# Performance work log

Hardware: AMD Instinct MI355X
Metric: run time of the kernel (lower is better)

The kernel has to match this reference:

```python
import jax, jax.numpy as jnp
import numpy as np


def setup_inputs() -> dict:
    key = jax.random.key(0)
    k1, k2, k3 = jax.random.split(key, 3)
    x = jax.random.normal(k1, (8, 3, 256, 256), dtype=jnp.float32)
    conv_w = jax.random.normal(k2, (64, 3), dtype=jnp.float32)  # 1x1 conv weight [O, C]
    w = jax.random.normal(k3, (64, 8), dtype=jnp.float32)       # per-channel LBP weights
    return {"x": x, "conv_w": conv_w, "w": w}


def _heaviside(d):
    # torch.heaviside(d, 0.): 1 where d > 0, else 0 (including d == 0)
    return jnp.where(d > 0, jnp.ones((), d.dtype), jnp.zeros((), d.dtype))


def reference(x, conv_w, w):
    # 1x1 conv, no bias: [N,C,H,W] x [O,C] -> [N,O,H,W]
    y = jnp.einsum('nchw,oc->nohw', x, conv_w)
    c = y[:, :, 1:-1, 1:-1]  # center, [N,O,H-2,W-2]
    # 8 neighbor shifts in the original order
    shifts = [
        y[:, :, 0:-2, 0:-2], y[:, :, 0:-2, 1:-1], y[:, :, 0:-2, 2:],
        y[:, :, 1:-1, 0:-2], y[:, :, 2:, 0:-2], y[:, :, 2:, 1:-1],
        y[:, :, 2:, 2:],    y[:, :, 1:-1, 2:],
    ]
    act = jnp.stack([_heaviside(c - s) for s in shifts], axis=2)  # [N,O,8,H-2,W-2]
    # weighted reduction over the 8 directions with exp(w)
    x_cat = jnp.einsum('nolhw,ol->nohw', act, jnp.exp(w))
    padded = jnp.pad(x_cat, ((0, 0), (0, 0), (1, 1), (1, 1)))  # ZeroPad2d(1)
    # res=True: concat raw input along channels -> [N, 3+O, H, W]
    return jnp.concatenate([x, padded], axis=1)
```

## Files before the change

kernel.cpp:

```cpp
#include <hip/hip_runtime.h>


__global__ __launch_bounds__(256) void lbp_all(
    const float* __restrict__ x,
    const float* __restrict__ conv_w,
    const float* __restrict__ w,
    float* __restrict__ out)
{
#pragma clang fp contract(off)
    const int n     = blockIdx.z;
    const int og    = blockIdx.y;
    const int tid   = threadIdx.x;
    const int lane  = tid & 63;
    const int wv    = tid >> 6;
    const int col   = lane * 4;
    const int hrow0 = blockIdx.x * 8 + wv * 2;

    __shared__ float ews[128];
    if (tid < 128) ews[tid] = expf(w[og * 128 + tid]);

    const float* xn = x + (size_t)n * 3 * 65536;

    float4 xr[4][3];
    #pragma unroll
    for (int r = 0; r < 4; ++r) {
        int row = hrow0 - 1 + r;
        row = row < 0 ? 0 : (row > 255 ? 255 : row);
        #pragma unroll
        for (int ch = 0; ch < 3; ++ch)
            xr[r][ch] = *(const float4*)(xn + (ch * 256 + row) * 256 + col);
    }

    if (og == 0) {
        #pragma unroll
        for (int ch = 0; ch < 3; ++ch) {
            float* cp = out + ((((size_t)n * 67 + ch) * 256 + hrow0) * 256 + col);
            *(float4*)cp         = xr[1][ch];
            *(float4*)(cp + 256) = xr[2][ch];
        }
    }

    __syncthreads();

    float* obase = out + ((((size_t)n * 67 + 3 + og * 16) * 256 + hrow0) * 256 + col);

    #pragma unroll 4
    for (int oi = 0; oi < 16; ++oi) {
        const int o = og * 16 + oi;
        const float cw0 = conv_w[o * 3 + 0];
        const float cw1 = conv_w[o * 3 + 1];
        const float cw2 = conv_w[o * 3 + 2];

        float Y[4][6];
        #pragma unroll
        for (int r = 0; r < 4; ++r) {
            float4 yv;
            yv.x = xr[r][0].x * cw0 + xr[r][1].x * cw1 + xr[r][2].x * cw2;
            yv.y = xr[r][0].y * cw0 + xr[r][1].y * cw1 + xr[r][2].y * cw2;
            yv.z = xr[r][0].z * cw0 + xr[r][1].z * cw1 + xr[r][2].z * cw2;
            yv.w = xr[r][0].w * cw0 + xr[r][1].w * cw1 + xr[r][2].w * cw2;
            Y[r][1] = yv.x; Y[r][2] = yv.y; Y[r][3] = yv.z; Y[r][4] = yv.w;
            Y[r][0] = __shfl_up(yv.w, 1);
            Y[r][5] = __shfl_down(yv.x, 1);
        }

        const float e0 = ews[oi * 8 + 0], e1 = ews[oi * 8 + 1];
        const float e2 = ews[oi * 8 + 2], e3 = ews[oi * 8 + 3];
        const float e4 = ews[oi * 8 + 4], e5 = ews[oi * 8 + 5];
        const float e6 = ews[oi * 8 + 6], e7 = ews[oi * 8 + 7];

        #pragma unroll
        for (int k = 0; k < 2; ++k) {
            const int hrow = hrow0 + k;
            float res[4];
            if (hrow == 0 || hrow == 255) {
                res[0] = res[1] = res[2] = res[3] = 0.f;
            } else {
                const float* up  = Y[k];
                const float* mid = Y[k + 1];
                const float* dn  = Y[k + 2];
                #pragma unroll
                for (int j = 0; j < 4; ++j) {
                    const float c = mid[j + 1];
                    float acc;
                    acc  = (c > up [j    ]) ? e0 : 0.f;
                    acc += (c > up [j + 1]) ? e1 : 0.f;
                    acc += (c > up [j + 2]) ? e2 : 0.f;
                    acc += (c > mid[j    ]) ? e3 : 0.f;
                    acc += (c > dn [j    ]) ? e4 : 0.f;
                    acc += (c > dn [j + 1]) ? e5 : 0.f;
                    acc += (c > dn [j + 2]) ? e6 : 0.f;
                    acc += (c > mid[j + 2]) ? e7 : 0.f;
                    res[j] = acc;
                }
                if (lane == 0)  res[0] = 0.f;
                if (lane == 63) res[3] = 0.f;
            }
            *(float4*)(obase + (size_t)oi * 65536 + (size_t)k * 256) =
                make_float4(res[0], res[1], res[2], res[3]);
        }
    }
}

extern "C" void kernel_launch(void* const* d_in, const int* in_sizes, int n_in,
                              void* d_out, int out_size, void* d_ws, size_t ws_size,
                              hipStream_t stream) {
    const float* x      = (const float*)d_in[0];
    const float* conv_w = (const float*)d_in[1];
    const float* w      = (const float*)d_in[2];
    float* out          = (float*)d_out;

    dim3 grid(32, 4, 8);
    dim3 block(256);
    hipLaunchKernelGGL(lbp_all, grid, block, 0, stream, x, conv_w, w, out);
}
```

Before: 152.0 us.

## Use nontemporal stores, halo loads instead of shuffles, and tune unroll/occupancy

```diff
diff --git a/kernel.cpp b/kernel.cpp
--- a/kernel.cpp
+++ b/kernel.cpp
@@ -1,7 +1,9 @@
 #include <hip/hip_runtime.h>
 
 
-__global__ __launch_bounds__(256) void lbp_all(
+typedef float vfloat4 __attribute__((ext_vector_type(4)));
+
+__global__ __launch_bounds__(256, 4) void lbp_all(
     const float* __restrict__ x,
     const float* __restrict__ conv_w,
     const float* __restrict__ w,
@@ -20,23 +22,30 @@
     if (tid < 128) ews[tid] = expf(w[og * 128 + tid]);
 
     const float* xn = x + (size_t)n * 3 * 65536;
+    const int cl = (col == 0)   ? 0   : col - 1;
+    const int cr = (col == 252) ? 255 : col + 4;
 
-    float4 xr[4][3];
+    vfloat4 xr[4][3];
+    float   hl[4][3], hr[4][3];
     #pragma unroll
     for (int r = 0; r < 4; ++r) {
         int row = hrow0 - 1 + r;
         row = row < 0 ? 0 : (row > 255 ? 255 : row);
         #pragma unroll
-        for (int ch = 0; ch < 3; ++ch)
-            xr[r][ch] = *(const float4*)(xn + (ch * 256 + row) * 256 + col);
+        for (int ch = 0; ch < 3; ++ch) {
+            const float* bp = xn + (ch * 256 + row) * 256;
+            xr[r][ch] = *(const vfloat4*)(bp + col);
+            hl[r][ch] = bp[cl];
+            hr[r][ch] = bp[cr];
+        }
     }
 
     if (og == 0) {
         #pragma unroll
         for (int ch = 0; ch < 3; ++ch) {
             float* cp = out + ((((size_t)n * 67 + ch) * 256 + hrow0) * 256 + col);
-            *(float4*)cp         = xr[1][ch];
-            *(float4*)(cp + 256) = xr[2][ch];
+            __builtin_nontemporal_store(xr[1][ch], (vfloat4*)cp);
+            __builtin_nontemporal_store(xr[2][ch], (vfloat4*)(cp + 256));
         }
     }
 
@@ -44,7 +53,7 @@
 
     float* obase = out + ((((size_t)n * 67 + 3 + og * 16) * 256 + hrow0) * 256 + col);
 
-    #pragma unroll 4
+    #pragma unroll 2
     for (int oi = 0; oi < 16; ++oi) {
         const int o = og * 16 + oi;
         const float cw0 = conv_w[o * 3 + 0];
@@ -54,20 +63,18 @@
         float Y[4][6];
         #pragma unroll
         for (int r = 0; r < 4; ++r) {
-            float4 yv;
-            yv.x = xr[r][0].x * cw0 + xr[r][1].x * cw1 + xr[r][2].x * cw2;
-            yv.y = xr[r][0].y * cw0 + xr[r][1].y * cw1 + xr[r][2].y * cw2;
-            yv.z = xr[r][0].z * cw0 + xr[r][1].z * cw1 + xr[r][2].z * cw2;
-            yv.w = xr[r][0].w * cw0 + xr[r][1].w * cw1 + xr[r][2].w * cw2;
-            Y[r][1] = yv.x; Y[r][2] = yv.y; Y[r][3] = yv.z; Y[r][4] = yv.w;
-            Y[r][0] = __shfl_up(yv.w, 1);
-            Y[r][5] = __shfl_down(yv.x, 1);
+            Y[r][0] = hl[r][0]   * cw0 + hl[r][1]   * cw1 + hl[r][2]   * cw2;
+            Y[r][1] = xr[r][0].x * cw0 + xr[r][1].x * cw1 + xr[r][2].x * cw2;
+            Y[r][2] = xr[r][0].y * cw0 + xr[r][1].y * cw1 + xr[r][2].y * cw2;
+            Y[r][3] = xr[r][0].z * cw0 + xr[r][1].z * cw1 + xr[r][2].z * cw2;
+            Y[r][4] = xr[r][0].w * cw0 + xr[r][1].w * cw1 + xr[r][2].w * cw2;
+            Y[r][5] = hr[r][0]   * cw0 + hr[r][1]   * cw1 + hr[r][2]   * cw2;
         }
 
-        const float e0 = ews[oi * 8 + 0], e1 = ews[oi * 8 + 1];
-        const float e2 = ews[oi * 8 + 2], e3 = ews[oi * 8 + 3];
-        const float e4 = ews[oi * 8 + 4], e5 = ews[oi * 8 + 5];
-        const float e6 = ews[oi * 8 + 6], e7 = ews[oi * 8 + 7];
+        const vfloat4 ev0 = *(const vfloat4*)&ews[oi * 8];
+        const vfloat4 ev1 = *(const vfloat4*)&ews[oi * 8 + 4];
+        const float e0 = ev0.x, e1 = ev0.y, e2 = ev0.z, e3 = ev0.w;
+        const float e4 = ev1.x, e5 = ev1.y, e6 = ev1.z, e7 = ev1.w;
 
         #pragma unroll
         for (int k = 0; k < 2; ++k) {
@@ -96,8 +103,9 @@
                 if (lane == 0)  res[0] = 0.f;
                 if (lane == 63) res[3] = 0.f;
             }
-            *(float4*)(obase + (size_t)oi * 65536 + (size_t)k * 256) =
-                make_float4(res[0], res[1], res[2], res[3]);
+            vfloat4 rv; rv.x = res[0]; rv.y = res[1]; rv.z = res[2]; rv.w = res[3];
+            __builtin_nontemporal_store(
+                rv, (vfloat4*)(obase + (size_t)oi * 65536 + (size_t)k * 256));
         }
     }
 }
```

Result: slower. 172.5 us (+13.5%).
